# Kernel tuning notes

Hardware: AMD Instinct MI355X
Metric: run time of the kernel (lower is better)

Reference implementation:

```python
import jax, jax.numpy as jnp
import numpy as np

VOCAB, NUM_TAGS, EMB, HID = 30000, 20, 200, 128
B, S = 128, 512


def setup_inputs() -> dict:
    key = jax.random.key(0)
    ks = jax.random.split(key, 13)
    sentence = jax.random.randint(ks[0], (B, S), 0, VOCAB)
    tags = jax.random.randint(ks[1], (B, S), 0, NUM_TAGS)
    lengths = jax.random.randint(ks[2], (B,), 1, S + 1)
    mask = jnp.arange(S)[None, :] < lengths[:, None]  # [B,S] bool, mask[:,0] all True
    sc = 0.1
    return {
        "sentence": sentence,
        "tags": tags,
        "mask": mask,
        "embedding": jax.random.normal(ks[3], (VOCAB, EMB), jnp.float32) * sc,
        "W_ih": jax.random.normal(ks[4], (4 * HID, EMB), jnp.float32) * sc,
        "W_hh": jax.random.normal(ks[5], (4 * HID, HID), jnp.float32) * sc,
        "b_ih": jax.random.normal(ks[6], (4 * HID,), jnp.float32) * sc,
        "b_hh": jax.random.normal(ks[7], (4 * HID,), jnp.float32) * sc,
        "W_dec": jax.random.normal(ks[8], (NUM_TAGS, HID), jnp.float32) * sc,
        "b_dec": jax.random.normal(ks[9], (NUM_TAGS,), jnp.float32) * sc,
        "start_trans": jax.random.normal(ks[10], (NUM_TAGS,), jnp.float32) * sc,
        "end_trans": jax.random.normal(ks[11], (NUM_TAGS,), jnp.float32) * sc,
        "trans": jax.random.normal(ks[12], (NUM_TAGS, NUM_TAGS), jnp.float32) * sc,
    }


def _lstm(embeds, W_ih, W_hh, b_ih, b_hh):
    # torch nn.LSTM, single layer, batch_first, zero init state; gate order i,f,g,o
    b = embeds.shape[0]
    h0 = jnp.zeros((b, HID), embeds.dtype)
    x = jnp.swapaxes(embeds, 0, 1)  # [S,B,E]
    xg = jnp.einsum('sbe,ge->sbg', x, W_ih) + b_ih + b_hh  # input projections, [S,B,4H]

    def step(carry, xg_t):
        h, c = carry
        g = xg_t + h @ W_hh.T
        i, f, gg, o = jnp.split(g, 4, axis=-1)
        c = jax.nn.sigmoid(f) * c + jax.nn.sigmoid(i) * jnp.tanh(gg)
        h = jax.nn.sigmoid(o) * jnp.tanh(c)
        return (h, c), h

    _, hs = jax.lax.scan(step, (h0, h0), xg)
    return jnp.swapaxes(hs, 0, 1)  # [B,S,H]


def _crf_nll_mean(emissions, tags, mask, start_trans, end_trans, trans):
    # torchcrf.CRF negative log likelihood, reduction='mean' (mean over batch)
    b = emissions.shape[0]
    ems = jnp.swapaxes(emissions, 0, 1)          # [S,B,T]
    tgs = jnp.swapaxes(tags, 0, 1)               # [S,B]
    msk = jnp.swapaxes(mask, 0, 1).astype(emissions.dtype)  # [S,B]
    bidx = jnp.arange(b)

    # numerator: score of the gold path
    num0 = start_trans[tgs[0]] + ems[0, bidx, tgs[0]]

    def nstep(score, inp):
        em, tag, ptag, m = inp
        return score + (trans[ptag, tag] + em[bidx, tag]) * m, None

    num, _ = jax.lax.scan(nstep, num0, (ems[1:], tgs[1:], tgs[:-1], msk[1:]))
    last_idx = mask.sum(axis=1).astype(jnp.int32) - 1
    num = num + end_trans[tags[bidx, last_idx]]

    # denominator: forward algorithm (log partition)
    sc0 = start_trans[None, :] + ems[0]  # [B,T]

    def dstep(score, inp):
        em, m = inp
        nxt = jax.nn.logsumexp(score[:, :, None] + trans[None] + em[:, None, :], axis=1)
        return jnp.where(m[:, None] > 0, nxt, score), None

    sc, _ = jax.lax.scan(dstep, sc0, (ems[1:], msk[1:]))
    den = jax.nn.logsumexp(sc + end_trans[None, :], axis=1)
    return -jnp.mean(num - den)


def reference(sentence, tags, mask, embedding, W_ih, W_hh, b_ih, b_hh,
              W_dec, b_dec, start_trans, end_trans, trans):
    embeds = embedding[sentence]                           # [B,S,E]
    lstm_out = _lstm(embeds, W_ih, W_hh, b_ih, b_hh)       # [B,S,H]
    emissions = jnp.einsum('bsh,th->bst', lstm_out, W_dec) + b_dec  # [B,S,T]
    # dropout treated as identity (eval-mode reference)
    return _crf_nll_mean(emissions, tags, mask, start_trans, end_trans, trans)
```

## Files before the change

### kernel.cpp

```cpp
#include <hip/hip_runtime.h>
#include <hip/hip_bf16.h>
#include <hip/hip_fp16.h>
#include <math.h>

#define B_ 128
#define S_ 512
#define EMB_ 200
#define HID_ 128
#define NT_ 20
#define G4_ 512
#define KP_ 224

typedef _Float16 f16x2_t __attribute__((ext_vector_type(2)));
typedef short bf16x8 __attribute__((ext_vector_type(8)));
typedef float f32x4 __attribute__((ext_vector_type(4)));

#if __has_builtin(__builtin_amdgcn_fdot2)
#define FDOT2(a, b, c) __builtin_amdgcn_fdot2(__builtin_bit_cast(f16x2_t, (a)), \
                                              __builtin_bit_cast(f16x2_t, (b)), (c), false)
#else
static __device__ __forceinline__ float fdot2_fb(unsigned a, unsigned b, float c) {
    float alo = __half2float(__ushort_as_half((unsigned short)(a & 0xffffu)));
    float ahi = __half2float(__ushort_as_half((unsigned short)(a >> 16)));
    float blo = __half2float(__ushort_as_half((unsigned short)(b & 0xffffu)));
    float bhi = __half2float(__ushort_as_half((unsigned short)(b >> 16)));
    return c + alo * blo + ahi * bhi;
}
#define FDOT2(a, b, c) fdot2_fb((a), (b), (c))
#endif

__device__ __forceinline__ float sigm_(float x) {
    x = fminf(fmaxf(x, -30.f), 30.f);
    float e = __expf(-x);
    return 1.f / (1.f + e);
}
__device__ __forceinline__ float tanh_(float x) {
    x = fminf(fmaxf(x, -15.f), 15.f);
    float e = __expf(2.f * x);
    return (e - 1.f) / (e + 1.f);
}
__device__ __forceinline__ float bf2f(unsigned u) {
    union { unsigned u; float f; } cv;
    cv.u = u << 16;
    return cv.f;
}
__device__ __forceinline__ unsigned packh2(float a, float b) {
    return ((unsigned)__half_as_ushort(__float2half(b)) << 16)
         | (unsigned)__half_as_ushort(__float2half(a));
}
__device__ __forceinline__ unsigned short f2bf(float f) {
    __hip_bfloat16 h = __float2bfloat16(f);
    unsigned short u;
    __builtin_memcpy(&u, &h, 2);
    return u;
}

__global__ void k_detect(const unsigned char* mask, int* flag) {
    __shared__ int partial[4];
    int tid = threadIdx.x;
    int s = 0;
    for (int i = tid; i < B_ * S_; i += 256) {
        if (i & 3) s += mask[i];
    }
    for (int m = 32; m >= 1; m >>= 1) s += __shfl_xor(s, m);
    if ((tid & 63) == 0) partial[tid >> 6] = s;
    __syncthreads();
    if (tid == 0) {
        int tot = partial[0] + partial[1] + partial[2] + partial[3];
        flag[0] = (tot > 0) ? 1 : 0;
    }
}

__global__ void k_prep(const float* __restrict__ W_ih, const float* __restrict__ b_ih,
                       const float* __restrict__ b_hh, __hip_bfloat16* __restrict__ Wb,
                       float* __restrict__ biasb) {
    int i = blockIdx.x * 256 + threadIdx.x;
    if (i < G4_ * KP_) {
        int g = i / KP_, k = i - g * KP_;
        float v = (k < EMB_) ? W_ih[g * EMB_ + k] : 0.f;
        Wb[i] = __float2bfloat16(v);
    }
    if (i < G4_) biasb[i] = b_ih[i] + b_hh[i];
}

__global__ __launch_bounds__(256, 2) void k_xg(const int* __restrict__ sentence,
                                               const float* __restrict__ embedding,
                                               const __hip_bfloat16* __restrict__ Wb,
                                               const float* __restrict__ biasb,
                                               __hip_bfloat16* __restrict__ xg) {
    __shared__ short Bl[G4_ * 40];
    __shared__ short Al[32 * 40];
    __shared__ int ids_s[32];
    int tid = threadIdx.x;
    int m0 = blockIdx.x * 32;
    int lane = tid & 63;
    int gbase = (tid >> 6) * 128;
    if (tid < 32) ids_s[tid] = sentence[m0 + tid];
    __syncthreads();

    f32x4 acc0[8], acc1[8];
#pragma unroll
    for (int n = 0; n < 8; n++) {
        acc0[n] = (f32x4){0.f, 0.f, 0.f, 0.f};
        acc1[n] = (f32x4){0.f, 0.f, 0.f, 0.f};
    }
    int lrow = lane & 15, lk = lane >> 4;

    for (int c = 0; c < 7; c++) {
        int k0 = c * 32;
#pragma unroll
        for (int i = 0; i < 8; i++) {
            int idx = tid + 256 * i;
            int row = idx >> 2, q = idx & 3;
            uint4 v = *(const uint4*)((const short*)Wb + (size_t)row * KP_ + k0 + q * 8);
            *(uint4*)(Bl + row * 40 + q * 8) = v;
        }
#pragma unroll
        for (int i = 0; i < 2; i++) {
            int j = tid + 256 * i;
            int row = j >> 4, kp = j & 15;
            int k = k0 + kp * 2;
            const float* e = embedding + (size_t)ids_s[row] * EMB_;
            float v0 = (k < EMB_) ? e[k] : 0.f;
            float v1 = (k + 1 < EMB_) ? e[k + 1] : 0.f;
            unsigned u = (unsigned)f2bf(v0) | ((unsigned)f2bf(v1) << 16);
            *(unsigned*)(Al + row * 40 + kp * 2) = u;
        }
        __syncthreads();
        bf16x8 a0 = *(const bf16x8*)(Al + lrow * 40 + lk * 8);
        bf16x8 a1 = *(const bf16x8*)(Al + (lrow + 16) * 40 + lk * 8);
#pragma unroll
        for (int n = 0; n < 8; n++) {
            bf16x8 bfr = *(const bf16x8*)(Bl + (gbase + n * 16 + lrow) * 40 + lk * 8);
            acc0[n] = __builtin_amdgcn_mfma_f32_16x16x32_bf16(a0, bfr, acc0[n], 0, 0, 0);
            acc1[n] = __builtin_amdgcn_mfma_f32_16x16x32_bf16(a1, bfr, acc1[n], 0, 0, 0);
        }
        __syncthreads();
    }
    int rbase = m0 + lk * 4;
#pragma unroll
    for (int n = 0; n < 8; n++) {
        int g = gbase + n * 16 + lrow;
        float bv = biasb[g];
#pragma unroll
        for (int r = 0; r < 4; r++) {
            xg[(size_t)(rbase + r) * G4_ + g] = __float2bfloat16(acc0[n][r] + bv);
            xg[(size_t)(rbase + r + 16) * G4_ + g] = __float2bfloat16(acc1[n][r] + bv);
        }
    }
}

__global__ __launch_bounds__(1024) __attribute__((amdgpu_waves_per_eu(4, 4)))
void k_lstm(const __hip_bfloat16* __restrict__ xg,
            const float* __restrict__ W_hh,
            unsigned* __restrict__ h2_out) {
    __shared__ unsigned h2_lds[64];
    __shared__ float part_lds[G4_];
    __shared__ float gate_lds[G4_];
    int b = blockIdx.x, tid = threadIdx.x;
    int wv = tid >> 6, lane = tid & 63;
    int p = wv >> 3;
    int g = ((wv & 7) << 6) | lane;

    unsigned w2[32];
    const float2* wrow = (const float2*)(W_hh + (size_t)g * HID_ + p * 64);
#pragma unroll
    for (int k = 0; k < 32; k++) {
        float2 f = wrow[k];
        w2[k] = packh2(f.x, f.y);
    }
#pragma unroll
    for (int k = 0; k < 32; k++) asm("" : "+v"(w2[k]));

    if (tid < 64) h2_lds[tid] = 0u;
    float c0 = 0.f, c1 = 0.f;
    const ushort* xgb = (const ushort*)(xg) + (size_t)b * S_ * G4_;
    unsigned* h2b = h2_out + (size_t)b * S_ * 64;
    __syncthreads();

    unsigned xr = (p == 0) ? (unsigned)xgb[g] : 0u;
    for (int t = 0; t < S_; t++) {
        unsigned xr_next = 0u;
        if (p == 0) {
            int tn = (t + 1 < S_) ? t + 1 : t;
            xr_next = xgb[(size_t)tn * G4_ + g];
        }
        float acc = 0.f;
        const uint4* hb4 = (const uint4*)(h2_lds + (p << 5));
#pragma unroll
        for (int q = 0; q < 8; q++) {
            uint4 hh = hb4[q];
            acc = FDOT2(w2[4 * q + 0], hh.x, acc);
            acc = FDOT2(w2[4 * q + 1], hh.y, acc);
            acc = FDOT2(w2[4 * q + 2], hh.z, acc);
            acc = FDOT2(w2[4 * q + 3], hh.w, acc);
        }
        if (p == 1) part_lds[g] = acc;
        __syncthreads();
        if (p == 0) {
            float pre = bf2f(xr) + acc + part_lds[g];
            int gt = g >> 7;
            float act = (gt == 2) ? tanh_(pre) : sigm_(pre);
            gate_lds[g] = act;
        }
        __syncthreads();
        if (tid < 64) {
            int j = tid;
            float2 iv = *(const float2*)(gate_lds + 2 * j);
            float2 fv = *(const float2*)(gate_lds + 128 + 2 * j);
            float2 gv = *(const float2*)(gate_lds + 256 + 2 * j);
            float2 ov = *(const float2*)(gate_lds + 384 + 2 * j);
            c0 = fv.x * c0 + iv.x * gv.x;
            c1 = fv.y * c1 + iv.y * gv.y;
            float h0 = ov.x * tanh_(c0);
            float h1 = ov.y * tanh_(c1);
            unsigned pk = packh2(h0, h1);
            h2_lds[j] = pk;
            h2b[(size_t)t * 64 + j] = pk;
        }
        __syncthreads();
        xr = xr_next;
    }
}

__global__ __launch_bounds__(320) void k_em(const unsigned* __restrict__ h2,
                                            const float* __restrict__ W_dec,
                                            const float* __restrict__ b_dec,
                                            float* __restrict__ em) {
    int half = threadIdx.x / 160;
    int r = threadIdx.x % 160;
    int tag = r >> 3, l8 = r & 7;
    const float* wd = W_dec + tag * HID_ + l8 * 16;
    float ws[16];
#pragma unroll
    for (int q = 0; q < 16; q++) ws[q] = wd[q];
    float bd = b_dec[tag];
    int row0 = blockIdx.x * 16 + half * 8;
    for (int rp = 0; rp < 8; rp++) {
        int row = row0 + rp;
        const uint4* h4 = (const uint4*)(h2 + (size_t)row * 64 + l8 * 8);
        uint4 a = h4[0], bq = h4[1];
        unsigned hv[8] = {a.x, a.y, a.z, a.w, bq.x, bq.y, bq.z, bq.w};
        float pacc = 0.f;
#pragma unroll
        for (int q = 0; q < 8; q++) {
            float lo = __half2float(__ushort_as_half((unsigned short)(hv[q] & 0xffffu)));
            float hi = __half2float(__ushort_as_half((unsigned short)(hv[q] >> 16)));
            pacc += lo * ws[2 * q] + hi * ws[2 * q + 1];
        }
        pacc += __shfl_xor(pacc, 1);
        pacc += __shfl_xor(pacc, 2);
        pacc += __shfl_xor(pacc, 4);
        if (l8 == 0) em[(size_t)row * NT_ + tag] = pacc + bd;
    }
}

__global__ __launch_bounds__(256, 2) void k_crf(const float* __restrict__ em,
                                                const int* __restrict__ tags,
                                                const void* __restrict__ mask,
                                                const int* __restrict__ flag,
                                                const float* __restrict__ start_trans,
                                                const float* __restrict__ end_trans,
                                                const float* __restrict__ trans,
                                                float* __restrict__ nll) {
    __shared__ float em_s[S_ * NT_];
    __shared__ float trans_s[NT_ * NT_];
    __shared__ float score[2][NT_];
    __shared__ int tags_s[S_];
    __shared__ unsigned char mask_s[S_];
    __shared__ float fin[NT_];
    __shared__ float num_sh;

    int b = blockIdx.x;
    int tid = threadIdx.x;
    const float* emb_ = em + (size_t)b * S_ * NT_;

    for (int i = tid; i < S_ * NT_; i += 256) em_s[i] = emb_[i];
    for (int i = tid; i < NT_ * NT_; i += 256) trans_s[i] = trans[i];
    for (int i = tid; i < S_; i += 256) tags_s[i] = tags[b * S_ + i];
    int fl = flag[0];
    for (int i = tid; i < S_; i += 256) {
        mask_s[i] = fl ? ((const unsigned char*)mask)[b * S_ + i]
                       : (unsigned char)(((const int*)mask)[b * S_ + i] != 0);
    }
    __syncthreads();
    if (tid < NT_) score[0][tid] = start_trans[tid] + em_s[tid];
    float num = 0.f;
    int lastTag = 0;
    if (tid == 192) {
        lastTag = tags_s[0];
        num = start_trans[lastTag] + em_s[lastTag];
    }
    __syncthreads();

    int tag = tid >> 3, l8 = tid & 7;
    int cur = 0;
    for (int t = 1; t < S_; t++) {
        if (tid < NT_ * 8) {
            float v0 = score[cur][l8] + trans_s[l8 * NT_ + tag];
            float v1 = score[cur][l8 + 8] + trans_s[(l8 + 8) * NT_ + tag];
            float v2 = (l8 < 4) ? score[cur][l8 + 16] + trans_s[(l8 + 16) * NT_ + tag]
                                : -INFINITY;
            float m = fmaxf(fmaxf(v0, v1), v2);
            m = fmaxf(m, __shfl_xor(m, 4));
            m = fmaxf(m, __shfl_xor(m, 2));
            m = fmaxf(m, __shfl_xor(m, 1));
            float s = __expf(v0 - m) + __expf(v1 - m) + ((l8 < 4) ? __expf(v2 - m) : 0.f);
            s += __shfl_xor(s, 4);
            s += __shfl_xor(s, 2);
            s += __shfl_xor(s, 1);
            if (l8 == 0) {
                float nxt = m + __logf(s) + em_s[t * NT_ + tag];
                score[cur ^ 1][tag] = mask_s[t] ? nxt : score[cur][tag];
            }
        }
        if (tid == 192) {
            if (mask_s[t]) {
                int tg = tags_s[t];
                num += trans_s[lastTag * NT_ + tg] + em_s[t * NT_ + tg];
                lastTag = tg;
            }
        }
        __syncthreads();
        cur ^= 1;
    }
    if (tid == 192) num_sh = num + end_trans[lastTag];
    if (tid < NT_) fin[tid] = score[cur][tid] + end_trans[tid];
    __syncthreads();
    if (tid == 0) {
        float m = fin[0];
#pragma unroll
        for (int i = 1; i < NT_; i++) m = fmaxf(m, fin[i]);
        float s = 0.f;
#pragma unroll
        for (int i = 0; i < NT_; i++) s += __expf(fin[i] - m);
        float den = m + __logf(s);
        nll[b] = den - num_sh;
    }
}

__global__ void k_final(const float* __restrict__ nll, float* __restrict__ out) {
    __shared__ float sums[2];
    int tid = threadIdx.x;
    float v = nll[tid];
    for (int m = 32; m >= 1; m >>= 1) v += __shfl_xor(v, m);
    if ((tid & 63) == 0) sums[tid >> 6] = v;
    __syncthreads();
    if (tid == 0) out[0] = (sums[0] + sums[1]) * (1.f / (float)B_);
}

extern "C" void kernel_launch(void* const* d_in, const int* in_sizes, int n_in,
                              void* d_out, int out_size, void* d_ws, size_t ws_size,
                              hipStream_t stream) {
    const int* sentence = (const int*)d_in[0];
    const int* tags = (const int*)d_in[1];
    const void* mask = d_in[2];
    const float* embedding = (const float*)d_in[3];
    const float* W_ih = (const float*)d_in[4];
    const float* W_hh = (const float*)d_in[5];
    const float* b_ih = (const float*)d_in[6];
    const float* b_hh = (const float*)d_in[7];
    const float* W_dec = (const float*)d_in[8];
    const float* b_dec = (const float*)d_in[9];
    const float* start_trans = (const float*)d_in[10];
    const float* end_trans = (const float*)d_in[11];
    const float* trans = (const float*)d_in[12];

    char* ws = (char*)d_ws;
    int* flag = (int*)ws;
    __hip_bfloat16* xg = (__hip_bfloat16*)(ws + 256);
    size_t off = 256 + (size_t)B_ * S_ * G4_ * 2;
    float* em = (float*)(ws + off);
    off += (size_t)B_ * S_ * NT_ * 4;
    float* nllp = (float*)(ws + off);
    off += 512;
    unsigned* h2_out = (unsigned*)(ws + off);
    off += (size_t)B_ * S_ * 64 * 4;
    __hip_bfloat16* Wb = (__hip_bfloat16*)(ws + off);
    off += (size_t)G4_ * KP_ * 2;
    float* biasb = (float*)(ws + off);

    k_detect<<<1, 256, 0, stream>>>((const unsigned char*)mask, flag);
    k_prep<<<(G4_ * KP_ + 255) / 256, 256, 0, stream>>>(W_ih, b_ih, b_hh, Wb, biasb);
    k_xg<<<(B_ * S_) / 32, 256, 0, stream>>>(sentence, embedding, Wb, biasb, xg);
    k_lstm<<<B_, 1024, 0, stream>>>(xg, W_hh, h2_out);
    k_em<<<(B_ * S_) / 16, 320, 0, stream>>>(h2_out, W_dec, b_dec, em);
    k_crf<<<B_, 256, 0, stream>>>(em, tags, mask, flag, start_trans, end_trans, trans, nllp);
    k_final<<<1, 128, 0, stream>>>(nllp, (float*)d_out);
}
```

Before: 788.1 us.

## Restructure LSTM step with wave-local gate exchange and double-buffered hidden state

The input-projection output is stored gate-interleaved per hidden unit, so each group of 8 lanes in a wave holds all four gates for one hidden element across two K-halves. Partial dot products are combined with a lane shuffle, gate activations are exchanged via shuffles, and the cell update runs in every lane. This drops the partial-sum and gate LDS buffers and two of the three barriers per timestep. Double buffering the hidden state lets a single barrier per step suffice. All lanes now load xg each step, and sigmoid/tanh use a clamped exp formulation.

```diff
diff --git a/kernel.cpp b/kernel.cpp
--- a/kernel.cpp
+++ b/kernel.cpp
@@ -142,10 +142,11 @@
     for (int n = 0; n < 8; n++) {
         int g = gbase + n * 16 + lrow;
         float bv = biasb[g];
+        int pos = ((g & 127) << 2) | (g >> 7);
 #pragma unroll
         for (int r = 0; r < 4; r++) {
-            xg[(size_t)(rbase + r) * G4_ + g] = __float2bfloat16(acc0[n][r] + bv);
-            xg[(size_t)(rbase + r + 16) * G4_ + g] = __float2bfloat16(acc1[n][r] + bv);
+            xg[(size_t)(rbase + r) * G4_ + pos] = __float2bfloat16(acc0[n][r] + bv);
+            xg[(size_t)(rbase + r + 16) * G4_ + pos] = __float2bfloat16(acc1[n][r] + bv);
         }
     }
 }
@@ -154,16 +155,15 @@
 void k_lstm(const __hip_bfloat16* __restrict__ xg,
             const float* __restrict__ W_hh,
             unsigned* __restrict__ h2_out) {
-    __shared__ unsigned h2_lds[64];
-    __shared__ float part_lds[G4_];
-    __shared__ float gate_lds[G4_];
+    __shared__ unsigned h2_lds[2][64];
     int b = blockIdx.x, tid = threadIdx.x;
     int wv = tid >> 6, lane = tid & 63;
-    int p = wv >> 3;
-    int g = ((wv & 7) << 6) | lane;
+    int el = lane >> 3, gt = (lane >> 1) & 3, half = lane & 1;
+    int e = (wv << 3) | el;
+    int g = (gt << 7) | e;
 
     unsigned w2[32];
-    const float2* wrow = (const float2*)(W_hh + (size_t)g * HID_ + p * 64);
+    const float2* wrow = (const float2*)(W_hh + (size_t)g * HID_ + half * 64);
 #pragma unroll
     for (int k = 0; k < 32; k++) {
         float2 f = wrow[k];
@@ -172,21 +172,21 @@
 #pragma unroll
     for (int k = 0; k < 32; k++) asm("" : "+v"(w2[k]));
 
-    if (tid < 64) h2_lds[tid] = 0u;
-    float c0 = 0.f, c1 = 0.f;
+    if (tid < 64) h2_lds[0][tid] = 0u;
+    float c = 0.f;
     const ushort* xgb = (const ushort*)(xg) + (size_t)b * S_ * G4_;
     unsigned* h2b = h2_out + (size_t)b * S_ * 64;
-    __syncthreads();
-
-    unsigned xr = (p == 0) ? (unsigned)xgb[g] : 0u;
+    int xpos = tid >> 1;
+    bool isg = (gt == 2);
+    __syncthreads();
+
+    unsigned xr = xgb[xpos];
     for (int t = 0; t < S_; t++) {
-        unsigned xr_next = 0u;
-        if (p == 0) {
-            int tn = (t + 1 < S_) ? t + 1 : t;
-            xr_next = xgb[(size_t)tn * G4_ + g];
-        }
+        int tn = (t + 1 < S_) ? t + 1 : t;
+        unsigned xr_next = xgb[(size_t)tn * G4_ + xpos];
+
         float acc = 0.f;
-        const uint4* hb4 = (const uint4*)(h2_lds + (p << 5));
+        const uint4* hb4 = (const uint4*)(h2_lds[t & 1] + (half << 5));
 #pragma unroll
         for (int q = 0; q < 8; q++) {
             uint4 hh = hb4[q];
@@ -195,28 +195,24 @@
             acc = FDOT2(w2[4 * q + 2], hh.z, acc);
             acc = FDOT2(w2[4 * q + 3], hh.w, acc);
         }
-        if (p == 1) part_lds[g] = acc;
-        __syncthreads();
-        if (p == 0) {
-            float pre = bf2f(xr) + acc + part_lds[g];
-            int gt = g >> 7;
-            float act = (gt == 2) ? tanh_(pre) : sigm_(pre);
-            gate_lds[g] = act;
-        }
-        __syncthreads();
-        if (tid < 64) {
-            int j = tid;
-            float2 iv = *(const float2*)(gate_lds + 2 * j);
-            float2 fv = *(const float2*)(gate_lds + 128 + 2 * j);
-            float2 gv = *(const float2*)(gate_lds + 256 + 2 * j);
-            float2 ov = *(const float2*)(gate_lds + 384 + 2 * j);
-            c0 = fv.x * c0 + iv.x * gv.x;
-            c1 = fv.y * c1 + iv.y * gv.y;
-            float h0 = ov.x * tanh_(c0);
-            float h1 = ov.y * tanh_(c1);
-            unsigned pk = packh2(h0, h1);
-            h2_lds[j] = pk;
-            h2b[(size_t)t * 64 + j] = pk;
+        acc += __shfl_xor(acc, 1);
+        float pre = bf2f(xr) + acc;
+        float xs = isg ? 2.f * pre : pre;
+        xs = fminf(fmaxf(xs, -30.f), 30.f);
+        float r = 1.f / (1.f + __expf(-xs));
+        float act = isg ? 2.f * r - 1.f : r;
+
+        float a1 = __shfl_xor(act, 2);
+        float a2 = __shfl_xor(act, 4);
+        float a3 = __shfl_xor(a1, 4);
+        c = a1 * c + act * a2;
+        float h = a3 * tanh_(c);
+        float hx = __shfl_xor(h, 8);
+        if ((lane & 15) == 0) {
+            unsigned pk = packh2(h, hx);
+            int pj = (wv << 2) | (el >> 1);
+            h2_lds[(t + 1) & 1][pj] = pk;
+            h2b[(size_t)t * 64 + pj] = pk;
         }
         __syncthreads();
         xr = xr_next;
```

Measured after the change: 824.7 us. 4.7% more time.

## Restructure CRF forward into single-wave per-tag lanes and parallelize numerator

Applied to the files above, without the earlier changes.

The CRF kernel now runs one 64-lane wave per sequence, with each lane owning one tag and keeping its transition column in registers. Each lane computes the logsumexp over all 20 predecessors with a register tree, replacing the 8-lane shuffle reductions. The gold-path numerator is computed in parallel across time with a wave reduction, where it was previously a serial per-step accumulation on one thread. LSTM gate activations are also merged into one sigmoid-based formula so tanh and sigmoid share a single exp path. Tradeoff: more per-lane work and higher register use per step, in exchange for fewer shuffles and cheaper barriers within a single wave.

```diff
diff --git a/kernel.cpp b/kernel.cpp
--- a/kernel.cpp
+++ b/kernel.cpp
@@ -29,16 +29,6 @@
 #define FDOT2(a, b, c) fdot2_fb((a), (b), (c))
 #endif
 
-__device__ __forceinline__ float sigm_(float x) {
-    x = fminf(fmaxf(x, -30.f), 30.f);
-    float e = __expf(-x);
-    return 1.f / (1.f + e);
-}
-__device__ __forceinline__ float tanh_(float x) {
-    x = fminf(fmaxf(x, -15.f), 15.f);
-    float e = __expf(2.f * x);
-    return (e - 1.f) / (e + 1.f);
-}
 __device__ __forceinline__ float bf2f(unsigned u) {
     union { unsigned u; float f; } cv;
     cv.u = u << 16;
@@ -200,8 +190,10 @@
         if (p == 0) {
             float pre = bf2f(xr) + acc + part_lds[g];
             int gt = g >> 7;
-            float act = (gt == 2) ? tanh_(pre) : sigm_(pre);
-            gate_lds[g] = act;
+            float xs = (gt == 2) ? 2.f * pre : pre;
+            xs = fminf(fmaxf(xs, -30.f), 30.f);
+            float r = 1.f / (1.f + __expf(-xs));
+            gate_lds[g] = (gt == 2) ? 2.f * r - 1.f : r;
         }
         __syncthreads();
         if (tid < 64) {
@@ -212,8 +204,8 @@
             float2 ov = *(const float2*)(gate_lds + 384 + 2 * j);
             c0 = fv.x * c0 + iv.x * gv.x;
             c1 = fv.y * c1 + iv.y * gv.y;
-            float h0 = ov.x * tanh_(c0);
-            float h1 = ov.y * tanh_(c1);
+            float h0 = ov.x * (2.f / (1.f + __expf(-2.f * c0)) - 1.f);
+            float h1 = ov.y * (2.f / (1.f + __expf(-2.f * c1)) - 1.f);
             unsigned pk = packh2(h0, h1);
             h2_lds[j] = pk;
             h2b[(size_t)t * 64 + j] = pk;
@@ -255,87 +247,102 @@
     }
 }
 
-__global__ __launch_bounds__(256, 2) void k_crf(const float* __restrict__ em,
-                                                const int* __restrict__ tags,
-                                                const void* __restrict__ mask,
-                                                const int* __restrict__ flag,
-                                                const float* __restrict__ start_trans,
-                                                const float* __restrict__ end_trans,
-                                                const float* __restrict__ trans,
-                                                float* __restrict__ nll) {
+__global__ __launch_bounds__(64) void k_crf(const float* __restrict__ em,
+                                            const int* __restrict__ tags,
+                                            const void* __restrict__ mask,
+                                            const int* __restrict__ flag,
+                                            const float* __restrict__ start_trans,
+                                            const float* __restrict__ end_trans,
+                                            const float* __restrict__ trans,
+                                            float* __restrict__ nll) {
     __shared__ float em_s[S_ * NT_];
     __shared__ float trans_s[NT_ * NT_];
-    __shared__ float score[2][NT_];
     __shared__ int tags_s[S_];
     __shared__ unsigned char mask_s[S_];
-    __shared__ float fin[NT_];
+    __shared__ __align__(16) float score_s[32];
     __shared__ float num_sh;
 
     int b = blockIdx.x;
-    int tid = threadIdx.x;
-    const float* emb_ = em + (size_t)b * S_ * NT_;
-
-    for (int i = tid; i < S_ * NT_; i += 256) em_s[i] = emb_[i];
-    for (int i = tid; i < NT_ * NT_; i += 256) trans_s[i] = trans[i];
-    for (int i = tid; i < S_; i += 256) tags_s[i] = tags[b * S_ + i];
+    int lane = threadIdx.x;
+    const float4* e4 = (const float4*)(em + (size_t)b * S_ * NT_);
+    float4* s4 = (float4*)em_s;
+    for (int i = lane; i < S_ * NT_ / 4; i += 64) s4[i] = e4[i];
+    for (int i = lane; i < NT_ * NT_; i += 64) trans_s[i] = trans[i];
+    for (int i = lane; i < S_; i += 64) tags_s[i] = tags[b * S_ + i];
     int fl = flag[0];
-    for (int i = tid; i < S_; i += 256) {
+    for (int i = lane; i < S_; i += 64) {
         mask_s[i] = fl ? ((const unsigned char*)mask)[b * S_ + i]
                        : (unsigned char)(((const int*)mask)[b * S_ + i] != 0);
     }
     __syncthreads();
-    if (tid < NT_) score[0][tid] = start_trans[tid] + em_s[tid];
-    float num = 0.f;
-    int lastTag = 0;
-    if (tid == 192) {
-        lastTag = tags_s[0];
-        num = start_trans[lastTag] + em_s[lastTag];
-    }
-    __syncthreads();
-
-    int tag = tid >> 3, l8 = tid & 7;
-    int cur = 0;
+
+    float nsum = 0.f;
+    int cnt = 0;
+    for (int t = lane; t < S_; t += 64) cnt += mask_s[t];
+    for (int t = 1 + lane; t < S_; t += 64) {
+        if (mask_s[t]) {
+            int tg = tags_s[t], pt = tags_s[t - 1];
+            nsum += trans_s[pt * NT_ + tg] + em_s[t * NT_ + tg];
+        }
+    }
+    for (int m = 32; m >= 1; m >>= 1) {
+        nsum += __shfl_xor(nsum, m);
+        cnt += __shfl_xor(cnt, m);
+    }
+    if (lane == 0) {
+        int t0 = tags_s[0];
+        num_sh = nsum + start_trans[t0] + em_s[t0] + end_trans[tags_s[cnt - 1]];
+    }
+
+    int tag = (lane < NT_) ? lane : NT_ - 1;
+    float tcol[NT_];
+#pragma unroll
+    for (int p = 0; p < NT_; p++) tcol[p] = trans_s[p * NT_ + tag];
+    float sc = start_trans[tag] + em_s[tag];
+    if (lane < NT_) score_s[lane] = sc;
+    __syncthreads();
+
     for (int t = 1; t < S_; t++) {
-        if (tid < NT_ * 8) {
-            float v0 = score[cur][l8] + trans_s[l8 * NT_ + tag];
-            float v1 = score[cur][l8 + 8] + trans_s[(l8 + 8) * NT_ + tag];
-            float v2 = (l8 < 4) ? score[cur][l8 + 16] + trans_s[(l8 + 16) * NT_ + tag]
-                                : -INFINITY;
-            float m = fmaxf(fmaxf(v0, v1), v2);
-            m = fmaxf(m, __shfl_xor(m, 4));
-            m = fmaxf(m, __shfl_xor(m, 2));
-            m = fmaxf(m, __shfl_xor(m, 1));
-            float s = __expf(v0 - m) + __expf(v1 - m) + ((l8 < 4) ? __expf(v2 - m) : 0.f);
-            s += __shfl_xor(s, 4);
-            s += __shfl_xor(s, 2);
-            s += __shfl_xor(s, 1);
-            if (l8 == 0) {
-                float nxt = m + __logf(s) + em_s[t * NT_ + tag];
-                score[cur ^ 1][tag] = mask_s[t] ? nxt : score[cur][tag];
-            }
-        }
-        if (tid == 192) {
-            if (mask_s[t]) {
-                int tg = tags_s[t];
-                num += trans_s[lastTag * NT_ + tg] + em_s[t * NT_ + tg];
-                lastTag = tg;
-            }
-        }
-        __syncthreads();
-        cur ^= 1;
-    }
-    if (tid == 192) num_sh = num + end_trans[lastTag];
-    if (tid < NT_) fin[tid] = score[cur][tid] + end_trans[tid];
-    __syncthreads();
-    if (tid == 0) {
-        float m = fin[0];
-#pragma unroll
-        for (int i = 1; i < NT_; i++) m = fmaxf(m, fin[i]);
+        const float4* q4 = (const float4*)score_s;
+        float4 q0 = q4[0], q1 = q4[1], q2 = q4[2], q3 = q4[3], q5 = q4[4];
+        float v[NT_] = {q0.x + tcol[0],  q0.y + tcol[1],  q0.z + tcol[2],  q0.w + tcol[3],
+                        q1.x + tcol[4],  q1.y + tcol[5],  q1.z + tcol[6],  q1.w + tcol[7],
+                        q2.x + tcol[8],  q2.y + tcol[9],  q2.z + tcol[10], q2.w + tcol[11],
+                        q3.x + tcol[12], q3.y + tcol[13], q3.z + tcol[14], q3.w + tcol[15],
+                        q5.x + tcol[16], q5.y + tcol[17], q5.z + tcol[18], q5.w + tcol[19]};
+        float mx[NT_];
+#pragma unroll
+        for (int p = 0; p < NT_; p++) mx[p] = v[p];
+#pragma unroll
+        for (int n = NT_; n > 1; n = (n + 1) >> 1) {
+#pragma unroll
+            for (int i = 0; i < (n >> 1); i++) mx[i] = fmaxf(mx[i], mx[n - 1 - i]);
+        }
+        float ex[NT_];
+#pragma unroll
+        for (int p = 0; p < NT_; p++) ex[p] = __expf(v[p] - mx[0]);
+#pragma unroll
+        for (int n = NT_; n > 1; n = (n + 1) >> 1) {
+#pragma unroll
+            for (int i = 0; i < (n >> 1); i++) ex[i] += ex[n - 1 - i];
+        }
+        float nxt = mx[0] + __logf(ex[0]) + em_s[t * NT_ + tag];
+        sc = mask_s[t] ? nxt : sc;
+        __syncthreads();
+        if (lane < NT_) score_s[lane] = sc;
+        __syncthreads();
+    }
+
+    if (lane < NT_) score_s[lane] = sc + end_trans[tag];
+    __syncthreads();
+    if (lane == 0) {
+        float m = score_s[0];
+#pragma unroll
+        for (int i = 1; i < NT_; i++) m = fmaxf(m, score_s[i]);
         float s = 0.f;
 #pragma unroll
-        for (int i = 0; i < NT_; i++) s += __expf(fin[i] - m);
-        float den = m + __logf(s);
-        nll[b] = den - num_sh;
+        for (int i = 0; i < NT_; i++) s += __expf(score_s[i] - m);
+        nll[b] = (m + __logf(s)) - num_sh;
     }
 }
 
@@ -385,6 +392,6 @@
     k_xg<<<(B_ * S_) / 32, 256, 0, stream>>>(sentence, embedding, Wb, biasb, xg);
     k_lstm<<<B_, 1024, 0, stream>>>(xg, W_hh, h2_out);
     k_em<<<(B_ * S_) / 16, 320, 0, stream>>>(h2_out, W_dec, b_dec, em);
-    k_crf<<<B_, 256, 0, stream>>>(em, tags, mask, flag, start_trans, end_trans, trans, nllp);
+    k_crf<<<B_, 64, 0, stream>>>(em, tags, mask, flag, start_trans, end_trans, trans, nllp);
     k_final<<<1, 128, 0, stream>>>(nllp, (float*)d_out);
 }
```

Measured after the change: 709.9 us. 9.9% less time.
